# Optimization experiments

Measured on AMD Instinct MI355X. Metric: run time of the kernel, lower is better.

## Reference

```python
import jax, jax.numpy as jnp
import numpy as np

N_HEAD = 12
HEAD_DIM = 64
EPS = 1e-6
ROPE_BASE = 10000.0


def rms_norm(x, w):
    x32 = x.astype(jnp.float32)
    var = jnp.mean(x32 * x32, axis=-1, keepdims=True)
    xn = x32 * jax.lax.rsqrt(var + EPS)
    return w * xn.astype(x.dtype)


def rotate_half(x):
    x1, x2 = jnp.split(x, 2, axis=-1)
    return jnp.concatenate((-x2, x1), axis=-1)


def rope_cos_sin(seq_len, dtype):
    inv_freq = 1.0 / (ROPE_BASE ** (jnp.arange(0, HEAD_DIM, 2, dtype=jnp.float32) / HEAD_DIM))
    pos = jnp.arange(seq_len, dtype=jnp.float32)
    freqs = pos[:, None] * inv_freq[None, :]          # [S, HEAD_DIM//2]
    emb = jnp.concatenate((freqs, freqs), axis=-1)    # [S, HEAD_DIM]
    # shape [1, 1, S, HEAD_DIM] (batch, head, seq, dim) after unsqueeze_dim=1
    return emb[None, None].astype(dtype), None  # placeholder, see below


def setup_inputs() -> dict:
    key = jax.random.key(0)
    ks = jax.random.split(key, 9)
    B, S, D, F = 1, 4096, 768, 2048
    s = 0.02
    return {
        "hidden_states": jax.random.normal(ks[0], (B, S, D), jnp.float32),
        "w_q": jax.random.normal(ks[1], (D, D), jnp.float32) * s,
        "w_k": jax.random.normal(ks[2], (D, D), jnp.float32) * s,
        "w_v": jax.random.normal(ks[3], (D, D), jnp.float32) * s,
        "w_o": jax.random.normal(ks[4], (D, D), jnp.float32) * s,
        "w_gate": jax.random.normal(ks[5], (D, F), jnp.float32) * s,
        "w_up": jax.random.normal(ks[6], (D, F), jnp.float32) * s,
        "w_down": jax.random.normal(ks[7], (F, D), jnp.float32) * s,
        "w_norm1": jnp.ones((D,), jnp.float32),
        "w_norm2": jnp.ones((D,), jnp.float32),
    }


def attention(x, w_q, w_k, w_v, w_o):
    B, S, D = x.shape
    scale = HEAD_DIM ** -0.5
    # project and split heads: [B, H, S, hd]
    q = (x @ w_q).reshape(B, S, N_HEAD, HEAD_DIM).transpose(0, 2, 1, 3)
    k = (x @ w_k).reshape(B, S, N_HEAD, HEAD_DIM).transpose(0, 2, 1, 3)
    v = (x @ w_v).reshape(B, S, N_HEAD, HEAD_DIM).transpose(0, 2, 1, 3)
    # rotary embedding (position_ids = arange(S))
    inv_freq = 1.0 / (ROPE_BASE ** (jnp.arange(0, HEAD_DIM, 2, dtype=jnp.float32) / HEAD_DIM))
    pos = jnp.arange(S, dtype=jnp.float32)
    freqs = pos[:, None] * inv_freq[None, :]
    emb = jnp.concatenate((freqs, freqs), axis=-1)          # [S, hd]
    cos = jnp.cos(emb).astype(x.dtype)[None, None]          # [1,1,S,hd]
    sin = jnp.sin(emb).astype(x.dtype)[None, None]
    q = q * cos + rotate_half(q) * sin
    k = k * cos + rotate_half(k) * sin
    # eager attention with causal mask (materialized, as in the original)
    scores = jnp.einsum("bhqd,bhkd->bhqk", q, k) * scale
    causal = jnp.triu(jnp.ones((S, S), dtype=bool), k=1)
    scores = jnp.where(causal, jnp.finfo(scores.dtype).min, scores)
    attn = jax.nn.softmax(scores.astype(jnp.float32), axis=-1).astype(q.dtype)
    out = jnp.einsum("bhqk,bhkd->bhqd", attn, v)
    out = out.transpose(0, 2, 1, 3).reshape(B, S, D)
    return out @ w_o


def reference(hidden_states, w_q, w_k, w_v, w_o, w_gate, w_up, w_down, w_norm1, w_norm2):
    x = hidden_states
    h = x + attention(rms_norm(x, w_norm1), w_q, w_k, w_v, w_o)
    y = rms_norm(h, w_norm2)
    ffn = (jax.nn.silu(y @ w_gate) * (y @ w_up)) @ w_down
    return h + ffn
```

## Files before the change

kernel.cpp:

```cpp
#include <hip/hip_runtime.h>
#include <hip/hip_bf16.h>

typedef __attribute__((ext_vector_type(8))) short s8v;
typedef __attribute__((ext_vector_type(4))) float f4v;
typedef __attribute__((ext_vector_type(16))) float f16v;
typedef __attribute__((ext_vector_type(4))) unsigned u4v;

typedef __attribute__((address_space(1))) const void as1_void;
typedef __attribute__((address_space(3))) void as3_void;

__device__ __forceinline__ void gl16(const void* g, void* l) {
  __builtin_amdgcn_global_load_lds((as1_void*)g, (as3_void*)l, 16, 0, 0);
}

__device__ __forceinline__ float b2f(int u) {
  union { float f; unsigned i; } c; c.i = ((unsigned)(u & 0xFFFF)) << 16; return c.f;
}
__device__ __forceinline__ unsigned short f2b(float f) {
  union { float f; unsigned i; } c; c.f = f;
  unsigned r = c.i + 0x7FFFu + ((c.i >> 16) & 1u);
  return (unsigned short)(r >> 16);
}
__device__ __forceinline__ unsigned pk2(float lo, float hi) {
  unsigned u;
  asm("v_cvt_pk_bf16_f32 %0, %1, %2" : "=v"(u) : "v"(lo), "v"(hi));
  return u;
}

#define MFMA16(a, b, c) __builtin_amdgcn_mfma_f32_16x16x32_bf16((a), (b), (c), 0, 0, 0)
#define MFMA32(a, b, c) __builtin_amdgcn_mfma_f32_32x32x16_bf16((a), (b), (c), 0, 0, 0)

struct Seg { const float* src; unsigned short* dst; int K; int N; int nbn; int nblocks; int mode; };
struct PrepArgs { Seg seg[9]; float* ct; float* st; const float* wn1; };

__global__ __launch_bounds__(256) void prep_k(PrepArgs a) {
  int b = blockIdx.x, si = 0;
  while (si < 8 && b >= a.seg[si].nblocks) { b -= a.seg[si].nblocks; ++si; }
  const Seg s = a.seg[si];
  const int tid = threadIdx.x;
  if (s.mode == 3) {
    const int t = b * 256 + tid;
    const int sq = t >> 5, d = t & 31;
    const float inv = powf(10000.0f, -(float)d * (1.0f / 32.0f));
    const float ang = (float)sq * inv;
    a.ct[t] = cosf(ang);
    a.st[t] = sinf(ang);
    return;
  }
  if (s.mode == 4) {
    const float* xr = s.src + (size_t)b * 768;
    float v0 = xr[tid], v1 = xr[tid + 256], v2 = xr[tid + 512];
    float ss = v0 * v0 + v1 * v1 + v2 * v2;
#pragma unroll
    for (int m = 1; m < 64; m <<= 1) ss += __shfl_xor(ss, m, 64);
    __shared__ float sred[4];
    if ((tid & 63) == 0) sred[tid >> 6] = ss;
    __syncthreads();
    const float tot = sred[0] + sred[1] + sred[2] + sred[3];
    const float rn = rsqrtf(tot * (1.0f / 768.0f) + 1e-6f);
    unsigned short* orow = s.dst + (size_t)b * 768;
    orow[tid]       = f2b(v0 * rn * a.wn1[tid]);
    orow[tid + 256] = f2b(v1 * rn * a.wn1[tid + 256]);
    orow[tid + 512] = f2b(v2 * rn * a.wn1[tid + 512]);
    return;
  }
  __shared__ float tile[32][33];
  const int tx = tid & 31, ty = tid >> 5;
  const int bn = b % s.nbn, bk = b / s.nbn;
#pragma unroll
  for (int i = 0; i < 32; i += 8)
    tile[ty + i][tx] = s.src[(size_t)(bk * 32 + ty + i) * s.N + bn * 32 + tx];
  __syncthreads();
#pragma unroll
  for (int i = 0; i < 32; i += 8) {
    int row;
    if (s.mode == 0)      row = bn * 32 + ty + i;
    else                  row = bn * 64 + (s.mode == 2 ? 32 : 0) + ty + i;
    s.dst[(size_t)row * s.K + bk * 32 + tx] = f2b(tile[tx][ty + i]);
  }
}

__global__ __launch_bounds__(256) void rmsnorm_k(const float* __restrict__ x,
    const float* __restrict__ w, unsigned short* __restrict__ out) {
  const int row = blockIdx.x, tid = threadIdx.x;
  const float* xr = x + (size_t)row * 768;
  float v0 = xr[tid], v1 = xr[tid + 256], v2 = xr[tid + 512];
  float ss = v0 * v0 + v1 * v1 + v2 * v2;
#pragma unroll
  for (int m = 1; m < 64; m <<= 1) ss += __shfl_xor(ss, m, 64);
  __shared__ float sred[4];
  if ((tid & 63) == 0) sred[tid >> 6] = ss;
  __syncthreads();
  const float tot = sred[0] + sred[1] + sred[2] + sred[3];
  const float rn = rsqrtf(tot * (1.0f / 768.0f) + 1e-6f);
  unsigned short* orow = out + (size_t)row * 768;
  orow[tid]       = f2b(v0 * rn * w[tid]);
  orow[tid + 256] = f2b(v1 * rn * w[tid + 256]);
  orow[tid + 512] = f2b(v2 * rn * w[tid + 512]);
}

template <int EPI, int BN>
__global__ __launch_bounds__(256) void gemm_bt(const unsigned short* __restrict__ A,
    const unsigned short* __restrict__ Bt, unsigned short* __restrict__ Cb,
    float* __restrict__ Cf, const float* __restrict__ R, int K, int ldc,
    const float* __restrict__ ct, const float* __restrict__ st) {
  constexpr int ABYTES = 128 * 32 * 2;
  constexpr int BBYTES = BN * 32 * 2;
  constexpr int MR = (BN == 128) ? 4 : 2;
  __shared__ unsigned short As[3 * 128 * 32];
  __shared__ unsigned short Bs[3 * BN * 32];
  const int tid = threadIdx.x;
  const int lane = tid & 63, wid = tid >> 6;
  const int wrow = (BN == 128) ? (wid >> 1) * 64 : wid * 32;
  const int wcol = (BN == 128) ? (wid & 1) * 64 : 0;
  const int l15 = lane & 15, l4 = lane >> 4;
  const int bm = blockIdx.y, bn = blockIdx.x;

  f4v acc[MR][4] = {};

  const int o0 = tid * 16, o1 = tid * 16 + 4096;
  const int r0 = o0 >> 6, c0 = o0 & 63;
  const int r1 = o1 >> 6, c1 = o1 & 63;
  const size_t ldab = (size_t)K * 2;
  const char* Abyte = (const char*)A;
  const char* Bbyte = (const char*)Bt;
  const size_t a0 = (size_t)(bm * 128 + r0) * ldab + c0;
  const size_t a1 = (size_t)(bm * 128 + r1) * ldab + c1;
  const size_t b0 = (size_t)(bn * BN + r0) * ldab + c0;
  const size_t b1 = (size_t)(bn * BN + r1) * ldab + c1;
  char* AsB = (char*)As;
  char* BsB = (char*)Bs;
  const int uoff = wid << 10;

#define STAGEK(I, SL) do { const size_t kb = (size_t)(I) * 64;                 \
    char* Aw = AsB + (SL) * ABYTES;                                            \
    char* Bw = BsB + (SL) * BBYTES;                                            \
    gl16(Abyte + a0 + kb, Aw + uoff);                                          \
    gl16(Abyte + a1 + kb, Aw + uoff + 4096);                                   \
    gl16(Bbyte + b0 + kb, Bw + uoff);                                          \
    if constexpr (BN == 128) gl16(Bbyte + b1 + kb, Bw + uoff + 4096); } while (0)

  const int NI = K >> 5;
  STAGEK(0, 0);
  STAGEK(1, 1);
  int sel = 0, nsl = 2;

  for (int i = 0; i < NI; ++i) {
    if (i < NI - 1) {
      if constexpr (BN == 128) asm volatile("s_waitcnt vmcnt(4)" ::: "memory");
      else                     asm volatile("s_waitcnt vmcnt(3)" ::: "memory");
    } else {
      asm volatile("s_waitcnt vmcnt(0)" ::: "memory");
    }
    __builtin_amdgcn_s_barrier();
    __builtin_amdgcn_sched_barrier(0);
    if (i + 2 < NI) STAGEK(i + 2, nsl);
    const char* Ar = AsB + sel * ABYTES;
    const char* Br = BsB + sel * BBYTES;
    s8v af[MR], bf[4];
#pragma unroll
    for (int m = 0; m < MR; ++m)
      af[m] = *(const s8v*)(Ar + (wrow + m * 16 + l15) * 64 + l4 * 16);
#pragma unroll
    for (int n = 0; n < 4; ++n)
      bf[n] = *(const s8v*)(Br + (wcol + n * 16 + l15) * 64 + l4 * 16);
    __builtin_amdgcn_s_setprio(1);
#pragma unroll
    for (int m = 0; m < MR; ++m)
#pragma unroll
      for (int n = 0; n < 4; ++n) acc[m][n] = MFMA16(af[m], bf[n], acc[m][n]);
    __builtin_amdgcn_s_setprio(0);
    sel = (sel == 2) ? 0 : sel + 1;
    nsl = (nsl == 2) ? 0 : nsl + 1;
  }
#undef STAGEK

  const int row0 = bm * 128 + wrow;
  const int col0 = bn * BN + wcol;

#pragma unroll
  for (int m = 0; m < MR; ++m)
#pragma unroll
    for (int n = 0; n < 4; ++n)
#pragma unroll
      for (int r = 0; r < 4; ++r) {
        const int row = row0 + m * 16 + l4 * 4 + r;
        const int col = col0 + n * 16 + l15;
        const float v = acc[m][n][r];
        if (EPI == 1) {
          Cf[(size_t)row * ldc + col] = v + R[(size_t)row * ldc + col];
        } else {
          Cb[(size_t)row * ldc + col] = f2b(v);
        }
      }
}

template <int EPI>
__global__ __launch_bounds__(512, 2) void gemm_big(const unsigned short* __restrict__ A,
    const unsigned short* __restrict__ Bt, unsigned short* __restrict__ Cb,
    int K, int ldc, const float* __restrict__ ct, const float* __restrict__ st) {
  constexpr int ABYTES = 256 * 32 * 2;
  constexpr int BBYTES = 128 * 32 * 2;
  __shared__ unsigned short As[3 * 256 * 32];
  __shared__ unsigned short Bs[3 * 128 * 32];
  const int tid = threadIdx.x;
  const int lane = tid & 63, wid = tid >> 6;
  const int wm = wid >> 1, wn = wid & 1;
  const int wrow = wm * 64, wcol = wn * 64;
  const int l15 = lane & 15, l4 = lane >> 4;
  const int bm = blockIdx.y, bn = blockIdx.x;

  f4v acc[4][4] = {};

  const size_t ldab = (size_t)K * 2;
  const char* Ab = (const char*)A;
  const char* Bb = (const char*)Bt;
  const int lrow = lane >> 2, lch = (lane & 3) * 16;
  const size_t aS0 = (size_t)(bm * 256 + wid * 16 + lrow) * ldab + lch;
  const size_t aS1 = (size_t)(bm * 256 + (wid + 8) * 16 + lrow) * ldab + lch;
  const size_t bS  = (size_t)(bn * 128 + wid * 16 + lrow) * ldab + lch;
  char* AsB = (char*)As;
  char* BsB = (char*)Bs;
  const int uA0 = wid << 10, uA1 = (wid + 8) << 10, uB = wid << 10;

#define STAGEK(I, SL) do { const size_t kb = (size_t)(I) * 64;                 \
    gl16(Ab + aS0 + kb, AsB + (SL) * ABYTES + uA0);                            \
    gl16(Ab + aS1 + kb, AsB + (SL) * ABYTES + uA1);                            \
    gl16(Bb + bS  + kb, BsB + (SL) * BBYTES + uB); } while (0)

  const int NI = K >> 5;
  STAGEK(0, 0);
  STAGEK(1, 1);
  int sel = 0, nsl = 2;

  for (int i = 0; i < NI; ++i) {
    if (i < NI - 1) asm volatile("s_waitcnt vmcnt(3)" ::: "memory");
    else            asm volatile("s_waitcnt vmcnt(0)" ::: "memory");
    __builtin_amdgcn_s_barrier();
    __builtin_amdgcn_sched_barrier(0);
    if (i + 2 < NI) STAGEK(i + 2, nsl);
    const char* Ar = AsB + sel * ABYTES;
    const char* Br = BsB + sel * BBYTES;
    s8v af[4], bf[4];
#pragma unroll
    for (int m = 0; m < 4; ++m)
      af[m] = *(const s8v*)(Ar + (wrow + m * 16 + l15) * 64 + l4 * 16);
#pragma unroll
    for (int n = 0; n < 4; ++n)
      bf[n] = *(const s8v*)(Br + (wcol + n * 16 + l15) * 64 + l4 * 16);
    __builtin_amdgcn_s_setprio(1);
#pragma unroll
    for (int m = 0; m < 4; ++m)
#pragma unroll
      for (int n = 0; n < 4; ++n) acc[m][n] = MFMA16(af[m], bf[n], acc[m][n]);
    __builtin_amdgcn_s_setprio(0);
    sel = (sel == 2) ? 0 : sel + 1;
    nsl = (nsl == 2) ? 0 : nsl + 1;
  }
#undef STAGEK

  const int row0 = bm * 256 + wrow;
  const int col0 = bn * 128 + wcol;

  if (EPI == 2 && bn < 12) {
#pragma unroll
    for (int m = 0; m < 4; ++m)
#pragma unroll
      for (int r = 0; r < 4; ++r) {
        const int row = row0 + m * 16 + l4 * 4 + r;
#pragma unroll
        for (int n = 0; n < 2; ++n) {
          const int d = n * 16 + l15;
          const float c  = ct[row * 32 + d];
          const float sn = st[row * 32 + d];
          const float aa = acc[m][n][r], bb = acc[m][n + 2][r];
          acc[m][n][r]     = aa * c - bb * sn;
          acc[m][n + 2][r] = bb * c + aa * sn;
        }
      }
  }
  if (EPI == 2 && bn < 6) {
    const float QSC = 0.18033688011112042f;
#pragma unroll
    for (int m = 0; m < 4; ++m)
#pragma unroll
      for (int n = 0; n < 4; ++n)
#pragma unroll
        for (int r = 0; r < 4; ++r) acc[m][n][r] *= QSC;
  }

  if (EPI == 3) {
    const int colb = (bn * 2 + wn) * 32;
#pragma unroll
    for (int m = 0; m < 4; ++m)
#pragma unroll
      for (int n = 0; n < 2; ++n)
#pragma unroll
        for (int r = 0; r < 4; ++r) {
          const int row = row0 + m * 16 + l4 * 4 + r;
          const float g = acc[m][n][r], u = acc[m][n + 2][r];
          const float val = g * u / (1.0f + __expf(-g));
          Cb[(size_t)row * 2048 + colb + n * 16 + l15] = f2b(val);
        }
    return;
  }

#pragma unroll
  for (int m = 0; m < 4; ++m)
#pragma unroll
    for (int n = 0; n < 4; ++n)
#pragma unroll
      for (int r = 0; r < 4; ++r) {
        const int row = row0 + m * 16 + l4 * 4 + r;
        const int col = col0 + n * 16 + l15;
        Cb[(size_t)row * ldc + col] = f2b(acc[m][n][r]);
      }
}

__global__ __launch_bounds__(256, 4) void flash_k(const unsigned short* __restrict__ qkv,
    uint2* __restrict__ Opart, float* __restrict__ ml) {
  const int kh = blockIdx.x, p = blockIdx.y, h = blockIdx.z;
  const int qbA = 63 - p;
  const int tid = threadIdx.x;
  const int wv = tid >> 6, lane = tid & 63;
  const int l31 = lane & 31, h8 = lane >> 5;
  const int myqb = (wv & 1) ? p : qbA;
  const int qrel = (wv >> 1) * 32 + l31;
  const int q_abs = myqb * 64 + qrel;

  __shared__ unsigned short Ks[2][64 * 72];
  __shared__ unsigned short Vt[2][64 * 72];

  const unsigned short* qp = qkv + h * 64;
  const unsigned short* kp = qkv + 768 + h * 64;
  const unsigned short* vp = qkv + 1536 + h * 64;

  s8v qf[4];
#pragma unroll
  for (int cc = 0; cc < 4; ++cc)
    qf[cc] = *(const s8v*)(qp + (size_t)q_abs * 2304 + cc * 16 + h8 * 8);

  f16v o0 = {}, o1 = {};
  float lp = 0.f;

  const int krow = tid >> 3, kc = (tid & 7) * 8;
  const int vj = tid & 31, vd0 = (tid >> 5) * 8;

  s8v ka, kb, va, vb;
#define LOADT(T) do { const size_t k0n = (size_t)(T) * 64;                    \
    ka = *(const s8v*)(kp + (k0n + krow) * 2304 + kc);                        \
    kb = *(const s8v*)(kp + (k0n + krow + 32) * 2304 + kc);                   \
    va = *(const s8v*)(vp + (k0n + 2 * vj) * 2304 + vd0);                     \
    vb = *(const s8v*)(vp + (k0n + 2 * vj + 1) * 2304 + vd0); } while (0)
#define WRITET(BUF) do {                                                      \
    *(s8v*)(Ks[BUF] + krow * 72 + kc) = ka;                                   \
    *(s8v*)(Ks[BUF] + (krow + 32) * 72 + kc) = kb;                            \
    unsigned* vtw = (unsigned*)(Vt[BUF] + (size_t)vd0 * 72 + 2 * vj);         \
    _Pragma("unroll")                                                         \
    for (int i = 0; i < 8; ++i)                                               \
      vtw[i * 36] = ((unsigned)(unsigned short)va[i]) |                       \
                    (((unsigned)(unsigned short)vb[i]) << 16); } while (0)

  LOADT(kh);
  WRITET(0);
  if (kh + 2 <= qbA) LOADT(kh + 2);
  __syncthreads();

  for (int t = kh; t <= qbA; t += 2) {
    const int cur = (t >> 1) & 1;
    if (t <= myqb) {
      f16v s0 = {}, s1 = {};
      __builtin_amdgcn_s_setprio(1);
#pragma unroll
      for (int cc = 0; cc < 4; ++cc) {
        const s8v kf0 = *(const s8v*)(Ks[cur] + l31 * 72 + cc * 16 + h8 * 8);
        const s8v kf1 = *(const s8v*)(Ks[cur] + (32 + l31) * 72 + cc * 16 + h8 * 8);
        s0 = MFMA32(kf0, qf[cc], s0);
        s1 = MFMA32(kf1, qf[cc], s1);
      }
      __builtin_amdgcn_s_setprio(0);
      if (t == myqb) {
#pragma unroll
        for (int rr = 0; rr < 16; ++rr) {
          const int koff = (rr & 3) + 8 * (rr >> 2) + 4 * h8;
          if (koff > qrel) s0[rr] = -1e30f;
          if (koff + 32 > qrel) s1[rr] = -1e30f;
        }
      }
#pragma unroll
      for (int rr = 0; rr < 16; ++rr) {
        s0[rr] = exp2f(s0[rr]);
        s1[rr] = exp2f(s1[rr]);
      }
      float sm[8];
#pragma unroll
      for (int i = 0; i < 8; ++i) sm[i] = (s0[i] + s0[i + 8]) + (s1[i] + s1[i + 8]);
#pragma unroll
      for (int i = 0; i < 4; ++i) sm[i] += sm[i + 4];
      lp += (sm[0] + sm[1]) + (sm[2] + sm[3]);

      unsigned pk0[8], pk1[8];
#pragma unroll
      for (int g = 0; g < 4; ++g)
#pragma unroll
        for (int j = 0; j < 2; ++j) {
          pk0[g * 2 + j] = pk2(s0[g * 4 + 2 * j], s0[g * 4 + 2 * j + 1]);
          pk1[g * 2 + j] = pk2(s1[g * 4 + 2 * j], s1[g * 4 + 2 * j + 1]);
        }
      __builtin_amdgcn_s_setprio(1);
#pragma unroll
      for (int cc = 0; cc < 4; ++cc) {
        const int g0 = (cc & 1) * 2, g1 = g0 + 1;
        const unsigned pA0 = (cc & 2) ? pk1[g0 * 2 + 0] : pk0[g0 * 2 + 0];
        const unsigned pA1 = (cc & 2) ? pk1[g0 * 2 + 1] : pk0[g0 * 2 + 1];
        const unsigned pB0 = (cc & 2) ? pk1[g1 * 2 + 0] : pk0[g1 * 2 + 0];
        const unsigned pB1 = (cc & 2) ? pk1[g1 * 2 + 1] : pk0[g1 * 2 + 1];
        const unsigned t00 = __shfl_xor((int)pA0, 32);
        const unsigned t01 = __shfl_xor((int)pA1, 32);
        const unsigned t10 = __shfl_xor((int)pB0, 32);
        const unsigned t11 = __shfl_xor((int)pB1, 32);
        union { u4v u; s8v s; } pf;
        pf.u[0] = h8 ? t10 : pA0;
        pf.u[1] = h8 ? t11 : pA1;
        pf.u[2] = h8 ? pB0 : t00;
        pf.u[3] = h8 ? pB1 : t01;
        const s8v vf0 = *(const s8v*)(Vt[cur] + l31 * 72 + cc * 16 + h8 * 8);
        const s8v vf1 = *(const s8v*)(Vt[cur] + (32 + l31) * 72 + cc * 16 + h8 * 8);
        o0 = MFMA32(vf0, pf.s, o0);
        o1 = MFMA32(vf1, pf.s, o1);
      }
      __builtin_amdgcn_s_setprio(0);
    }
    if (t + 2 <= qbA) {
      WRITET(cur ^ 1);
      if (t + 4 <= qbA) LOADT(t + 4);
      __syncthreads();
    }
  }

  lp += __shfl_xor(lp, 32);

  const size_t obase = ((size_t)kh * 12 + h) * 16 * 4096;
#pragma unroll
  for (int g = 0; g < 4; ++g) {
    const uint2 v0 = make_uint2(pk2(o0[g * 4], o0[g * 4 + 1]), pk2(o0[g * 4 + 2], o0[g * 4 + 3]));
    const uint2 v1 = make_uint2(pk2(o1[g * 4], o1[g * 4 + 1]), pk2(o1[g * 4 + 2], o1[g * 4 + 3]));
    Opart[obase + (size_t)(2 * g + h8) * 4096 + q_abs] = v0;
    Opart[obase + (size_t)(8 + 2 * g + h8) * 4096 + q_abs] = v1;
  }
  if (h8 == 0)
    ml[((size_t)kh * 12 + h) * 4096 + q_abs] = lp;
#undef LOADT
#undef WRITET
}

__global__ __launch_bounds__(256) void combine_k(const uint2* __restrict__ Opart,
    const float* __restrict__ ml, unsigned short* __restrict__ out) {
  const int u = blockIdx.x * 256 + threadIdx.x;
  const int q = u & 4095;
  const int rest = u >> 12;
  const int dgrp = rest & 15;
  const int h = rest >> 4;
  const float l0 = ml[h * 4096 + q];
  const float l1 = ml[12 * 4096 + h * 4096 + q];
  const float inv = 1.0f / (l0 + l1);
  const size_t idx = ((size_t)h * 16 + dgrp) * 4096 + q;
  const uint2 a = Opart[idx];
  const uint2 b = Opart[(size_t)12 * 16 * 4096 + idx];
  const int dbase = (dgrp < 8) ? 4 * dgrp : 32 + 4 * (dgrp - 8);
  ushort4 r;
  r.x = f2b((b2f(a.x) + b2f(b.x)) * inv);
  r.y = f2b((b2f(a.x >> 16) + b2f(b.x >> 16)) * inv);
  r.z = f2b((b2f(a.y) + b2f(b.y)) * inv);
  r.w = f2b((b2f(a.y >> 16) + b2f(b.y >> 16)) * inv);
  *(ushort4*)(out + (size_t)q * 768 + h * 64 + dbase) = r;
}

extern "C" void kernel_launch(void* const* d_in, const int* in_sizes, int n_in,
                              void* d_out, int out_size, void* d_ws, size_t ws_size,
                              hipStream_t stream) {
  const float* x    = (const float*)d_in[0];
  const float* w_q  = (const float*)d_in[1];
  const float* w_k  = (const float*)d_in[2];
  const float* w_v  = (const float*)d_in[3];
  const float* w_o  = (const float*)d_in[4];
  const float* w_g  = (const float*)d_in[5];
  const float* w_u  = (const float*)d_in[6];
  const float* w_d  = (const float*)d_in[7];
  const float* w_n1 = (const float*)d_in[8];
  const float* w_n2 = (const float*)d_in[9];
  (void)in_sizes; (void)n_in; (void)out_size; (void)ws_size;

  char* ws = (char*)d_ws;
  size_t off = 0;
  auto alloc = [&](size_t bytes) { char* p = ws + off; off += (bytes + 255) & ~(size_t)255; return p; };
  unsigned short* wqkvT = (unsigned short*)alloc(2304ull * 768 * 2);
  unsigned short* woT   = (unsigned short*)alloc(768ull * 768 * 2);
  unsigned short* wguT  = (unsigned short*)alloc(4096ull * 768 * 2);
  unsigned short* wdT   = (unsigned short*)alloc(768ull * 2048 * 2);
  float* ct             = (float*)alloc(4096ull * 32 * 4);
  float* st             = (float*)alloc(4096ull * 32 * 4);
  unsigned short* xn    = (unsigned short*)alloc(4096ull * 768 * 2);
  unsigned short* qkv   = (unsigned short*)alloc(4096ull * 2304 * 2);
  unsigned short* attn  = (unsigned short*)alloc(4096ull * 768 * 2);
  float* hbuf           = (float*)alloc(4096ull * 768 * 4);
  unsigned short* ybuf  = (unsigned short*)alloc(4096ull * 768 * 2);
  unsigned short* ffn   = (unsigned short*)alloc(4096ull * 2048 * 2);
  uint2* Opart          = (uint2*)alloc(2ull * 12 * 16 * 4096 * 8);
  float* mlb            = (float*)alloc(2ull * 12 * 4096 * 4);

  PrepArgs pa;
  pa.seg[0] = { w_q, wqkvT,                 768,  768, 24,  576, 0 };
  pa.seg[1] = { w_k, wqkvT + 768 * 768,     768,  768, 24,  576, 0 };
  pa.seg[2] = { w_v, wqkvT + 2 * 768 * 768, 768,  768, 24,  576, 0 };
  pa.seg[3] = { w_o, woT,                   768,  768, 24,  576, 0 };
  pa.seg[4] = { w_g, wguT,                  768, 2048, 64, 1536, 1 };
  pa.seg[5] = { w_u, wguT,                  768, 2048, 64, 1536, 2 };
  pa.seg[6] = { w_d, wdT,                  2048,  768, 24, 1536, 0 };
  pa.seg[7] = { nullptr, nullptr, 0, 0, 0, 512, 3 };
  pa.seg[8] = { x, xn, 0, 0, 0, 4096, 4 };
  pa.ct = ct; pa.st = st; pa.wn1 = w_n1;
  const int prep_blocks = 576 * 4 + 1536 * 3 + 512 + 4096;

  prep_k<<<prep_blocks, 256, 0, stream>>>(pa);
  gemm_big<2><<<dim3(18, 16), 512, 0, stream>>>(xn, wqkvT, qkv, 768, 2304, ct, st);
  flash_k<<<dim3(2, 32, 12), 256, 0, stream>>>(qkv, Opart, mlb);
  combine_k<<<3072, 256, 0, stream>>>(Opart, mlb, attn);
  gemm_bt<1, 64><<<dim3(12, 32), 256, 0, stream>>>(attn, woT, nullptr, hbuf, x, 768, 768, nullptr, nullptr);
  rmsnorm_k<<<4096, 256, 0, stream>>>(hbuf, w_n2, ybuf);
  gemm_big<3><<<dim3(32, 16), 512, 0, stream>>>(ybuf, wguT, ffn, 768, 2048, nullptr, nullptr);
  gemm_bt<1, 64><<<dim3(12, 32), 256, 0, stream>>>(ffn, wdT, nullptr, (float*)d_out, hbuf, 2048, 768, nullptr, nullptr);
}
```

Before: 216.2 us.

## Load K fragments directly to registers and use permlane32 swap in flash kernel

The flash attention kernel no longer stages K tiles through shared memory. Each wave loads its K MFMA fragments straight from global memory into registers and prefetches the next tile after the QK MFMAs. The cross-half exchange of P fragments now uses v_permlane32_swap instead of four shuffles plus selects. Occupancy hint drops from 4 to 3 blocks per CU to make room for the extra register pressure, at the cost of less latency hiding and duplicated K global loads across waves. The unconditional LOADV(kh+2) may read past the valid tile range.

Result: slower. 229.9 us (+6.3%).

```diff
diff --git a/kernel.cpp b/kernel.cpp
--- a/kernel.cpp
+++ b/kernel.cpp
@@ -317,7 +317,7 @@
       }
 }
 
-__global__ __launch_bounds__(256, 4) void flash_k(const unsigned short* __restrict__ qkv,
+__global__ __launch_bounds__(256, 3) void flash_k(const unsigned short* __restrict__ qkv,
     uint2* __restrict__ Opart, float* __restrict__ ml) {
   const int kh = blockIdx.x, p = blockIdx.y, h = blockIdx.z;
   const int qbA = 63 - p;
@@ -328,7 +328,6 @@
   const int qrel = (wv >> 1) * 32 + l31;
   const int q_abs = myqb * 64 + qrel;
 
-  __shared__ unsigned short Ks[2][64 * 72];
   __shared__ unsigned short Vt[2][64 * 72];
 
   const unsigned short* qp = qkv + h * 64;
@@ -343,27 +342,30 @@
   f16v o0 = {}, o1 = {};
   float lp = 0.f;
 
-  const int krow = tid >> 3, kc = (tid & 7) * 8;
   const int vj = tid & 31, vd0 = (tid >> 5) * 8;
 
-  s8v ka, kb, va, vb;
-#define LOADT(T) do { const size_t k0n = (size_t)(T) * 64;                    \
-    ka = *(const s8v*)(kp + (k0n + krow) * 2304 + kc);                        \
-    kb = *(const s8v*)(kp + (k0n + krow + 32) * 2304 + kc);                   \
+  s8v kf0[4], kf1[4];
+  s8v va, vb;
+#define LOADK(T) do { const size_t krr = (size_t)(T) * 64 + l31;              \
+    _Pragma("unroll")                                                         \
+    for (int c2 = 0; c2 < 4; ++c2) {                                          \
+      kf0[c2] = *(const s8v*)(kp + krr * 2304 + c2 * 16 + h8 * 8);            \
+      kf1[c2] = *(const s8v*)(kp + (krr + 32) * 2304 + c2 * 16 + h8 * 8);     \
+    } } while (0)
+#define LOADV(T) do { const size_t k0n = (size_t)(T) * 64;                    \
     va = *(const s8v*)(vp + (k0n + 2 * vj) * 2304 + vd0);                     \
     vb = *(const s8v*)(vp + (k0n + 2 * vj + 1) * 2304 + vd0); } while (0)
 #define WRITET(BUF) do {                                                      \
-    *(s8v*)(Ks[BUF] + krow * 72 + kc) = ka;                                   \
-    *(s8v*)(Ks[BUF] + (krow + 32) * 72 + kc) = kb;                            \
     unsigned* vtw = (unsigned*)(Vt[BUF] + (size_t)vd0 * 72 + 2 * vj);         \
     _Pragma("unroll")                                                         \
     for (int i = 0; i < 8; ++i)                                               \
       vtw[i * 36] = ((unsigned)(unsigned short)va[i]) |                       \
                     (((unsigned)(unsigned short)vb[i]) << 16); } while (0)
 
-  LOADT(kh);
+  LOADK(kh);
+  LOADV(kh);
   WRITET(0);
-  if (kh + 2 <= qbA) LOADT(kh + 2);
+  LOADV(kh + 2);
   __syncthreads();
 
   for (int t = kh; t <= qbA; t += 2) {
@@ -373,12 +375,11 @@
       __builtin_amdgcn_s_setprio(1);
 #pragma unroll
       for (int cc = 0; cc < 4; ++cc) {
-        const s8v kf0 = *(const s8v*)(Ks[cur] + l31 * 72 + cc * 16 + h8 * 8);
-        const s8v kf1 = *(const s8v*)(Ks[cur] + (32 + l31) * 72 + cc * 16 + h8 * 8);
-        s0 = MFMA32(kf0, qf[cc], s0);
-        s1 = MFMA32(kf1, qf[cc], s1);
+        s0 = MFMA32(kf0[cc], qf[cc], s0);
+        s1 = MFMA32(kf1[cc], qf[cc], s1);
       }
       __builtin_amdgcn_s_setprio(0);
+      if (t + 2 <= myqb) LOADK(t + 2);
       if (t == myqb) {
 #pragma unroll
         for (int rr = 0; rr < 16; ++rr) {
@@ -411,19 +412,17 @@
 #pragma unroll
       for (int cc = 0; cc < 4; ++cc) {
         const int g0 = (cc & 1) * 2, g1 = g0 + 1;
-        const unsigned pA0 = (cc & 2) ? pk1[g0 * 2 + 0] : pk0[g0 * 2 + 0];
-        const unsigned pA1 = (cc & 2) ? pk1[g0 * 2 + 1] : pk0[g0 * 2 + 1];
-        const unsigned pB0 = (cc & 2) ? pk1[g1 * 2 + 0] : pk0[g1 * 2 + 0];
-        const unsigned pB1 = (cc & 2) ? pk1[g1 * 2 + 1] : pk0[g1 * 2 + 1];
-        const unsigned t00 = __shfl_xor((int)pA0, 32);
-        const unsigned t01 = __shfl_xor((int)pA1, 32);
-        const unsigned t10 = __shfl_xor((int)pB0, 32);
-        const unsigned t11 = __shfl_xor((int)pB1, 32);
+        unsigned a0 = (cc & 2) ? pk1[g0 * 2 + 0] : pk0[g0 * 2 + 0];
+        unsigned a1 = (cc & 2) ? pk1[g0 * 2 + 1] : pk0[g0 * 2 + 1];
+        unsigned b0 = (cc & 2) ? pk1[g1 * 2 + 0] : pk0[g1 * 2 + 0];
+        unsigned b1 = (cc & 2) ? pk1[g1 * 2 + 1] : pk0[g1 * 2 + 1];
+        asm("v_permlane32_swap_b32 %0, %1" : "+v"(a0), "+v"(b0));
+        asm("v_permlane32_swap_b32 %0, %1" : "+v"(a1), "+v"(b1));
         union { u4v u; s8v s; } pf;
-        pf.u[0] = h8 ? t10 : pA0;
-        pf.u[1] = h8 ? t11 : pA1;
-        pf.u[2] = h8 ? pB0 : t00;
-        pf.u[3] = h8 ? pB1 : t01;
+        pf.u[0] = a0;
+        pf.u[1] = a1;
+        pf.u[2] = b0;
+        pf.u[3] = b1;
         const s8v vf0 = *(const s8v*)(Vt[cur] + l31 * 72 + cc * 16 + h8 * 8);
         const s8v vf1 = *(const s8v*)(Vt[cur] + (32 + l31) * 72 + cc * 16 + h8 * 8);
         o0 = MFMA32(vf0, pf.s, o0);
@@ -433,7 +432,7 @@
     }
     if (t + 2 <= qbA) {
       WRITET(cur ^ 1);
-      if (t + 4 <= qbA) LOADT(t + 4);
+      if (t + 4 <= qbA) LOADV(t + 4);
       __syncthreads();
     }
   }
@@ -450,7 +449,8 @@
   }
   if (h8 == 0)
     ml[((size_t)kh * 12 + h) * 4096 + q_abs] = lp;
-#undef LOADT
+#undef LOADK
+#undef LOADV
 #undef WRITET
 }
 
```
